# Performance work log

Measured on AMD Instinct MI355X. Metric: run time of the kernel, lower is better.

## Reference

```python
import jax, jax.numpy as jnp
import numpy as np

N, C, K = 65536, 128, 16

def setup_inputs() -> dict:
    key = jax.random.key(0)
    ks = jax.random.split(key, 16)
    def w(k, i, o):
        return jax.random.normal(k, (i, o), dtype=jnp.float32) / np.sqrt(i)
    inp = {
        "x": jax.random.normal(ks[0], (N, C), dtype=jnp.float32),
        "coords": jax.random.normal(ks[1], (N, 3), dtype=jnp.float32) * 10.0,
        "neighbor_idx": jax.random.randint(ks[2], (N, K), 0, N, dtype=jnp.int32),
        # linear_top / linear_down (1x1 Minkowski convs, BN folded into affine)
        "W_top": w(ks[3], C, C), "b_top": jnp.zeros((C,), jnp.float32),
        "W_down": w(ks[4], C, C), "b_down": jnp.zeros((C,), jnp.float32),
        # phi (query), psi (key), alpha (value) 1x1 convs
        "W_phi": w(ks[5], C, C), "b_phi": jnp.zeros((C,), jnp.float32),
        "W_psi": w(ks[6], C, C), "b_psi": jnp.zeros((C,), jnp.float32),
        "W_alpha": w(ks[7], C, C), "b_alpha": jnp.zeros((C,), jnp.float32),
        # delta: positional-encoding MLP on relative xyz (3 -> C -> C)
        "W_d1": w(ks[8], 3, C), "b_d1": jnp.zeros((C,), jnp.float32),
        "W_d2": w(ks[9], C, C), "b_d2": jnp.zeros((C,), jnp.float32),
        # gamma: attention MLP (C -> C -> C), vector attention
        "W_g1": w(ks[10], C, C), "b_g1": jnp.zeros((C,), jnp.float32),
        "W_g2": w(ks[11], C, C), "b_g2": jnp.zeros((C,), jnp.float32),
    }
    return inp

def reference(x, coords, W_top, b_top, W_down, b_down, W_phi, b_phi, W_psi, b_psi,
              W_alpha, b_alpha, W_d1, b_d1, W_d2, b_d2, W_g1, b_g1, W_g2, b_g2,
              neighbor_idx):
    # linear_top
    h = x @ W_top + b_top                                  # (N, C)
    phi = h @ W_phi + b_phi                                # (N, C) query
    psi = h @ W_psi + b_psi                                # (N, C) key
    alpha = h @ W_alpha + b_alpha                          # (N, C) value
    # gather neighbor features / coords (irregular access)
    nb_psi = psi[neighbor_idx]                             # (N, K, C)
    nb_alpha = alpha[neighbor_idx]                         # (N, K, C)
    rel = coords[:, None, :] - coords[neighbor_idx]        # (N, K, 3)
    # delta: relative positional encoding MLP
    pos = jax.nn.relu(rel @ W_d1 + b_d1) @ W_d2 + b_d2     # (N, K, C)
    # vector attention: gamma(phi_i - psi_j + delta)
    attn_in = phi[:, None, :] - nb_psi + pos               # (N, K, C)
    logits = jax.nn.relu(attn_in @ W_g1 + b_g1) @ W_g2 + b_g2
    w = jax.nn.softmax(logits, axis=1)                     # softmax over K neighbors
    y = jnp.sum(w * (nb_alpha + pos), axis=1)              # (N, C)
    # linear_down + residual
    return y @ W_down + b_down + x
```

## Files before the change

kernel.cpp:

```cpp
#include <hip/hip_runtime.h>
#include <math.h>

#define C 128
#define K 16
#define M 4
#define ROWS 64

typedef unsigned short ushort_t;
typedef unsigned int u32;
typedef float f32x4 __attribute__((ext_vector_type(4)));
typedef _Float16 f16x8 __attribute__((ext_vector_type(8)));

union U8h { _Float16 h[8]; uint4 u; };

__device__ __forceinline__ float f16tof(ushort_t b) {
    _Float16 h = __builtin_bit_cast(_Float16, b); return (float)h;
}
__device__ __forceinline__ ushort_t ftof16(float f) {
    _Float16 h = (_Float16)f; return __builtin_bit_cast(ushort_t, h);
}
__device__ __forceinline__ f32x4 mfma16(f16x8 a, f16x8 b, f32x4 c) {
    return __builtin_amdgcn_mfma_f32_16x16x32_f16(a, b, c, 0, 0, 0);
}

__global__ __launch_bounds__(128) void k_prep(
    const float* __restrict__ s0, const float* __restrict__ s1,
    const float* __restrict__ s2, const float* __restrict__ s3,
    ushort_t* __restrict__ d0, ushort_t* __restrict__ d1,
    ushort_t* __restrict__ d2, ushort_t* __restrict__ d3)
{
    const int m = blockIdx.x >> 7, n = blockIdx.x & 127, e = threadIdx.x;
    const float* s = (m==0) ? s0 : (m==1) ? s1 : (m==2) ? s2 : s3;
    ushort_t*   d = (m==0) ? d0 : (m==1) ? d1 : (m==2) ? d2 : d3;
    d[n*C + e] = ftof16(s[e*C + n]);
}

__global__ __launch_bounds__(512) void k_qkv2(
    const float* __restrict__ x,
    const ushort_t* __restrict__ WTt, const float* __restrict__ bt,
    const ushort_t* __restrict__ WTp, const float* __restrict__ bp,
    const ushort_t* __restrict__ WTs, const float* __restrict__ bs,
    const ushort_t* __restrict__ WTa, const float* __restrict__ ba,
    ushort_t* __restrict__ phiB, ushort_t* __restrict__ psiB,
    ushort_t* __restrict__ alfB)
{
    __shared__ ushort_t sX[64*C];
    __shared__ ushort_t sH[64*C];
    const int tid = threadIdx.x, lane = tid & 63, wv = tid >> 6;
    const int ncol = (wv<<4) + (lane&15), arow = lane&15;
    const int kgrp = lane>>4, krow0 = kgrp<<3;
    const int r0 = blockIdx.x * 64;

    {
        const int rX = tid>>3, cX = (tid&7)<<4;
        const float* xp = &x[(size_t)(r0+rX)*C + cX];
        #pragma unroll
        for (int hf = 0; hf < 2; ++hf) {
            const float4 a  = *(const float4*)&xp[hf*8 + 0];
            const float4 b2 = *(const float4*)&xp[hf*8 + 4];
            U8h v;
            v.h[0]=(_Float16)a.x;  v.h[1]=(_Float16)a.y;
            v.h[2]=(_Float16)a.z;  v.h[3]=(_Float16)a.w;
            v.h[4]=(_Float16)b2.x; v.h[5]=(_Float16)b2.y;
            v.h[6]=(_Float16)b2.z; v.h[7]=(_Float16)b2.w;
            const int col = cX + hf*8;
            *(uint4*)&sX[(rX<<7) + (col ^ ((rX&7)<<3))] = v.u;
        }
    }
    __syncthreads();

    {
        f16x8 bf[4]; f32x4 hacc[4];
        #pragma unroll
        for (int kk = 0; kk < 4; ++kk)
            bf[kk] = *(const f16x8*)&WTt[(size_t)ncol*C + (kk<<5) + krow0];
        #pragma unroll
        for (int m = 0; m < 4; ++m) hacc[m] = (f32x4){0.f,0.f,0.f,0.f};
        __builtin_amdgcn_s_setprio(1);
        #pragma unroll
        for (int m = 0; m < 4; ++m)
            #pragma unroll
            for (int kk = 0; kk < 4; ++kk) {
                const int row = (m<<4) + arow;
                const f16x8 af = *(const f16x8*)&sX[(row<<7) + (((kk<<5)+krow0) ^ ((arow&7)<<3))];
                hacc[m] = mfma16(af, bf[kk], hacc[m]);
            }
        __builtin_amdgcn_s_setprio(0);
        const float btc = bt[ncol];
        #pragma unroll
        for (int m = 0; m < 4; ++m)
            #pragma unroll
            for (int r = 0; r < 4; ++r) {
                const int row = (m<<4) + (kgrp<<2) + r;
                const u32 hv = ftof16(hacc[m][r] + btc);
                const u32 pv = (u32)__shfl_xor((int)hv, 1);
                if (!(lane&1))
                    *(u32*)&sH[(row<<7) + (ncol ^ ((row&7)<<3))] = hv | (pv<<16);
            }
    }
    __syncthreads();

#define OGEMM(WT_, b_, o_)                                                    \
    {                                                                         \
        f16x8 wf[4]; f32x4 oacc[4];                                           \
        _Pragma("unroll")                                                     \
        for (int kk = 0; kk < 4; ++kk)                                        \
            wf[kk] = *(const f16x8*)&WT_[(size_t)ncol*C + (kk<<5) + krow0];   \
        _Pragma("unroll")                                                     \
        for (int m = 0; m < 4; ++m) oacc[m] = (f32x4){0.f,0.f,0.f,0.f};      \
        __builtin_amdgcn_s_setprio(1);                                        \
        _Pragma("unroll")                                                     \
        for (int m = 0; m < 4; ++m)                                           \
            _Pragma("unroll")                                                 \
            for (int kk = 0; kk < 4; ++kk) {                                  \
                const int row = (m<<4) + arow;                                \
                const f16x8 af = *(const f16x8*)&sH[(row<<7) + (((kk<<5)+krow0) ^ ((arow&7)<<3))]; \
                oacc[m] = mfma16(af, wf[kk], oacc[m]);                        \
            }                                                                 \
        __builtin_amdgcn_s_setprio(0);                                        \
        const float bc = b_[ncol];                                            \
        _Pragma("unroll")                                                     \
        for (int m = 0; m < 4; ++m)                                           \
            _Pragma("unroll")                                                 \
            for (int r = 0; r < 4; ++r) {                                     \
                const int row = (m<<4) + (kgrp<<2) + r;                       \
                const u32 hv = ftof16(oacc[m][r] + bc);                       \
                const u32 pv = (u32)__shfl_xor((int)hv, 1);                   \
                if (!(lane&1))                                                \
                    *(u32*)&o_[(size_t)(r0+row)*C + ncol] = hv | (pv<<16);    \
            }                                                                 \
    }
    OGEMM(WTp, bp, phiB)
    OGEMM(WTs, bs, psiB)
    OGEMM(WTa, ba, alfB)
#undef OGEMM
}

__global__ __launch_bounds__(512, 2) void k_attn5(
    const ushort_t* __restrict__ phiB, const ushort_t* __restrict__ psiB,
    const ushort_t* __restrict__ alfB,
    const float* __restrict__ coords, const int* __restrict__ nidx,
    const float* __restrict__ Wd1, const float* __restrict__ bd1,
    const ushort_t* __restrict__ WTd2, const float* __restrict__ bd2,
    const ushort_t* __restrict__ WTg1, const float* __restrict__ bg1,
    const ushort_t* __restrict__ WTg2,
    const ushort_t* __restrict__ WTdn, const float* __restrict__ bdn,
    const float* __restrict__ x, float* __restrict__ out,
    int ngroups, int gpb)
{
    __shared__ ushort_t sT0[ROWS*C];
    __shared__ ushort_t sT1[ROWS*C];
    __shared__ ushort_t sA[ROWS*C];
    __shared__ float    sWd1[3][C];
    __shared__ float    sbd1v[C];
    __shared__ float    sY[M][C];

    const int tid  = threadIdx.x, lane = tid & 63, wv = tid >> 6;
    const int ncol = (wv<<4) + (lane&15);
    const int arow = lane & 15;
    const int kgrp = lane >> 4, krow0 = kgrp << 3;
    const int grow = tid >> 3;
    const int gpt  = grow >> 4;
    const int gk   = grow & 15;
    const int gc   = (tid & 7) << 4;

    const int g0 = blockIdx.x * gpb;
    if (g0 >= ngroups) return;
    const int gend = (g0 + gpb < ngroups) ? (g0 + gpb) : ngroups;

    if (tid < 3*C) ((float*)sWd1)[tid] = Wd1[tid];
    else if (tid < 4*C) sbd1v[tid - 3*C] = bd1[tid - 3*C];

    f16x8 wd2[4], wg1[4], wg2[4], wdn[4];
    #pragma unroll
    for (int kk = 0; kk < 4; ++kk) {
        wd2[kk] = *(const f16x8*)&WTd2[(size_t)ncol*C + (kk<<5) + krow0];
        wg1[kk] = *(const f16x8*)&WTg1[(size_t)ncol*C + (kk<<5) + krow0];
        wg2[kk] = *(const f16x8*)&WTg2[(size_t)ncol*C + (kk<<5) + krow0];
        wdn[kk] = *(const f16x8*)&WTdn[(size_t)ncol*C + (kgrp<<5) + (kk<<3)];
    }
    const float bd2c = bd2[ncol], bg1c = bg1[ncol], bdnc = bdn[ncol];

    __syncthreads();

    int jP; float cn0,cn1,cn2,cj0,cj1,cj2;
    {
        const int pt = g0*M + gpt;
        jP  = nidx[(size_t)pt*K + gk];
        cn0 = coords[(size_t)pt*3+0]; cn1 = coords[(size_t)pt*3+1]; cn2 = coords[(size_t)pt*3+2];
        cj0 = coords[(size_t)jP*3+0]; cj1 = coords[(size_t)jP*3+1]; cj2 = coords[(size_t)jP*3+2];
    }

    const int si0 = (grow<<7) + (gc ^ ((grow&7)<<3));
    const int si1 = (grow<<7) + ((gc+8) ^ ((grow&7)<<3));

    for (int g = g0; g < gend; ++g) {
        const int p0 = g * M;
        const bool hn = (g + 1 < gend);

        {
            const float rx = cn0 - cj0, ry = cn1 - cj1, rz = cn2 - cj2;
            #pragma unroll
            for (int hf = 0; hf < 2; ++hf) {
                U8h hi, lo;
                #pragma unroll
                for (int z = 0; z < 8; ++z) {
                    const int c = gc + (hf<<3) + z;
                    float t = fmaf(rx, sWd1[0][c],
                              fmaf(ry, sWd1[1][c],
                              fmaf(rz, sWd1[2][c], sbd1v[c])));
                    t = fmaxf(t, 0.f);
                    hi.h[z] = (_Float16)t;
                    lo.h[z] = (_Float16)(t - (float)hi.h[z]);
                }
                const int si = hf ? si1 : si0;
                *(uint4*)&sT0[si] = hi.u;
                *(uint4*)&sT1[si] = lo.u;
            }
        }
        __syncthreads();

        ushort_t phv[M];
        ushort_t psv[M][4];
        #pragma unroll
        for (int m = 0; m < M; ++m) {
            phv[m] = phiB[(size_t)(p0+m)*C + ncol];
            #pragma unroll
            for (int r = 0; r < 4; ++r) {
                const int j = nidx[(size_t)(p0+m)*K + (kgrp<<2) + r];
                psv[m][r] = psiB[(size_t)j*C + ncol];
            }
        }

        f32x4 pos[M];
        #pragma unroll
        for (int m = 0; m < M; ++m) pos[m] = (f32x4){0.f,0.f,0.f,0.f};
        __builtin_amdgcn_s_setprio(1);
        #pragma unroll
        for (int m = 0; m < M; ++m)
            #pragma unroll
            for (int kk = 0; kk < 4; ++kk) {
                const int si = (((m<<4)+arow)<<7) + (((kk<<5)+krow0) ^ ((arow&7)<<3));
                pos[m] = mfma16(*(const f16x8*)&sT0[si], wd2[kk], pos[m]);
                pos[m] = mfma16(*(const f16x8*)&sT1[si], wd2[kk], pos[m]);
            }
        __builtin_amdgcn_s_setprio(0);

        #pragma unroll
        for (int m = 0; m < M; ++m) {
            #pragma unroll
            for (int z = 0; z < 4; ++z) pos[m][z] += bd2c;
            const float phic = f16tof(phv[m]);
            #pragma unroll
            for (int r = 0; r < 4; ++r) {
                const int row = (m<<4) + (kgrp<<2) + r;
                const float av = phic - f16tof(psv[m][r]) + pos[m][r];
                const u32 hv = ftof16(av);
                const u32 hp = (u32)__shfl_xor((int)hv, 1);
                if (!(lane&1)) {
                    const int si = (row<<7) + (ncol ^ ((row&7)<<3));
                    *(u32*)&sA[si] = hv | (hp<<16);
                }
            }
        }
        __syncthreads();

        ushort_t alv[M][4];
        #pragma unroll
        for (int m = 0; m < M; ++m)
            #pragma unroll
            for (int r = 0; r < 4; ++r) {
                const int j = nidx[(size_t)(p0+m)*K + (kgrp<<2) + r];
                alv[m][r] = alfB[(size_t)j*C + ncol];
            }

        {
            f32x4 ua[M];
            #pragma unroll
            for (int m = 0; m < M; ++m) ua[m] = (f32x4){0.f,0.f,0.f,0.f};
            __builtin_amdgcn_s_setprio(1);
            #pragma unroll
            for (int m = 0; m < M; ++m)
                #pragma unroll
                for (int kk = 0; kk < 4; ++kk) {
                    const int si = (((m<<4)+arow)<<7) + (((kk<<5)+krow0) ^ ((arow&7)<<3));
                    ua[m] = mfma16(*(const f16x8*)&sA[si], wg1[kk], ua[m]);
                }
            __builtin_amdgcn_s_setprio(0);
            #pragma unroll
            for (int m = 0; m < M; ++m)
                #pragma unroll
                for (int r = 0; r < 4; ++r) {
                    const int row = (m<<4) + (kgrp<<2) + r;
                    const u32 hv = ftof16(fmaxf(ua[m][r] + bg1c, 0.f));
                    const u32 hp = (u32)__shfl_xor((int)hv, 1);
                    if (!(lane&1)) {
                        const int si = (row<<7) + (ncol ^ ((row&7)<<3));
                        *(u32*)&sT1[si] = hv | (hp<<16);
                    }
                }
        }
        if (hn) {
            const int pt = (g+1)*M + gpt;
            jP  = nidx[(size_t)pt*K + gk];
            cn0 = coords[(size_t)pt*3+0]; cn1 = coords[(size_t)pt*3+1]; cn2 = coords[(size_t)pt*3+2];
            cj0 = coords[(size_t)jP*3+0]; cj1 = coords[(size_t)jP*3+1]; cj2 = coords[(size_t)jP*3+2];
        }
        __syncthreads();

        f32x4 lg[M];
        #pragma unroll
        for (int m = 0; m < M; ++m) lg[m] = (f32x4){0.f,0.f,0.f,0.f};
        __builtin_amdgcn_s_setprio(1);
        #pragma unroll
        for (int m = 0; m < M; ++m)
            #pragma unroll
            for (int kk = 0; kk < 4; ++kk) {
                const int si = (((m<<4)+arow)<<7) + (((kk<<5)+krow0) ^ ((arow&7)<<3));
                lg[m] = mfma16(*(const f16x8*)&sT1[si], wg2[kk], lg[m]);
            }
        __builtin_amdgcn_s_setprio(0);

        #pragma unroll
        for (int m = 0; m < M; ++m) {
            float mx = fmaxf(fmaxf(lg[m][0], lg[m][1]), fmaxf(lg[m][2], lg[m][3]));
            mx = fmaxf(mx, __shfl_xor(mx, 16));
            mx = fmaxf(mx, __shfl_xor(mx, 32));
            const float e0 = __expf(lg[m][0]-mx), e1 = __expf(lg[m][1]-mx);
            const float e2 = __expf(lg[m][2]-mx), e3 = __expf(lg[m][3]-mx);
            float den = e0 + e1 + e2 + e3;
            den += __shfl_xor(den, 16);
            den += __shfl_xor(den, 32);
            const float inv = 1.0f / den;
            float yp;
            yp  = e0 * (f16tof(alv[m][0]) + pos[m][0]);
            yp += e1 * (f16tof(alv[m][1]) + pos[m][1]);
            yp += e2 * (f16tof(alv[m][2]) + pos[m][2]);
            yp += e3 * (f16tof(alv[m][3]) + pos[m][3]);
            yp *= inv;
            yp += __shfl_xor(yp, 16);
            yp += __shfl_xor(yp, 32);
            if (lane < 16) sY[m][ncol] = yp;
        }
        __syncthreads();

        #pragma unroll
        for (int m = 0; m < M; ++m) {
            float acc = 0.f;
            const int e0i = kgrp << 5;
            #pragma unroll
            for (int z = 0; z < 4; ++z) {
                const float4 ya = *(const float4*)&sY[m][e0i + (z<<3)];
                const float4 yb = *(const float4*)&sY[m][e0i + (z<<3) + 4];
                const f16x8 w8 = wdn[z];
                acc = fmaf(ya.x, (float)w8[0], acc);
                acc = fmaf(ya.y, (float)w8[1], acc);
                acc = fmaf(ya.z, (float)w8[2], acc);
                acc = fmaf(ya.w, (float)w8[3], acc);
                acc = fmaf(yb.x, (float)w8[4], acc);
                acc = fmaf(yb.y, (float)w8[5], acc);
                acc = fmaf(yb.z, (float)w8[6], acc);
                acc = fmaf(yb.w, (float)w8[7], acc);
            }
            acc += __shfl_xor(acc, 16);
            acc += __shfl_xor(acc, 32);
            if (lane < 16) {
                const size_t p = (size_t)(p0 + m);
                out[p*C + ncol] = acc + bdnc + x[p*C + ncol];
            }
        }
    }
}

extern "C" void kernel_launch(void* const* d_in, const int* in_sizes, int n_in,
                              void* d_out, int out_size, void* d_ws, size_t ws_size,
                              hipStream_t stream)
{
    const float* x      = (const float*)d_in[0];
    const float* coords = (const float*)d_in[1];
    const int*   nidx   = (const int*)d_in[2];
    const float* W_top  = (const float*)d_in[3];
    const float* b_top  = (const float*)d_in[4];
    const float* W_down = (const float*)d_in[5];
    const float* b_down = (const float*)d_in[6];
    const float* W_phi  = (const float*)d_in[7];
    const float* b_phi  = (const float*)d_in[8];
    const float* W_psi  = (const float*)d_in[9];
    const float* b_psi  = (const float*)d_in[10];
    const float* W_alpha= (const float*)d_in[11];
    const float* b_alpha= (const float*)d_in[12];
    const float* W_d1   = (const float*)d_in[13];
    const float* b_d1   = (const float*)d_in[14];
    const float* W_d2   = (const float*)d_in[15];
    const float* b_d2   = (const float*)d_in[16];
    const float* W_g1   = (const float*)d_in[17];
    const float* b_g1   = (const float*)d_in[18];
    const float* W_g2   = (const float*)d_in[19];
    const float* b_g2   = (const float*)d_in[20];
    (void)b_g2;

    const int N = in_sizes[0] / C;

    ushort_t* WTt  = (ushort_t*)d_ws;
    ushort_t* WTp  = WTt  + C*C;
    ushort_t* WTs  = WTp  + C*C;
    ushort_t* WTa  = WTs  + C*C;
    ushort_t* WTd2 = WTa  + C*C;
    ushort_t* WTg1 = WTd2 + C*C;
    ushort_t* WTg2 = WTg1 + C*C;
    ushort_t* WTdn = WTg2 + C*C;
    ushort_t* phiB = WTdn + C*C;
    ushort_t* psiB = phiB + (size_t)N*C;
    ushort_t* alfB = psiB + (size_t)N*C;
    float* out = (float*)d_out;

    hipLaunchKernelGGL(k_prep, dim3(4*C), dim3(C), 0, stream,
        W_top, W_phi, W_psi, W_alpha, WTt, WTp, WTs, WTa);
    hipLaunchKernelGGL(k_prep, dim3(4*C), dim3(C), 0, stream,
        W_d2, W_g1, W_g2, W_down, WTd2, WTg1, WTg2, WTdn);

    hipLaunchKernelGGL(k_qkv2, dim3(N / 64), dim3(512), 0, stream,
        x, WTt, b_top, WTp, b_phi, WTs, b_psi, WTa, b_alpha,
        phiB, psiB, alfB);

    const int ngroups = N / M;
    const int NBLK = 2048;
    const int gpb = (ngroups + NBLK - 1) / NBLK;
    hipLaunchKernelGGL(k_attn5, dim3(NBLK), dim3(512), 0, stream,
        phiB, psiB, alfB, coords, nidx,
        W_d1, b_d1, WTd2, b_d2, WTg1, b_g1, WTg2,
        WTdn, b_down, x, out, ngroups, gpb);
}
```

Before: 634.4 us.

## Split down-projection into separate MFMA kernel to cut attention kernel registers

```diff
diff --git a/kernel.cpp b/kernel.cpp
--- a/kernel.cpp
+++ b/kernel.cpp
@@ -92,10 +92,7 @@
             #pragma unroll
             for (int r = 0; r < 4; ++r) {
                 const int row = (m<<4) + (kgrp<<2) + r;
-                const u32 hv = ftof16(hacc[m][r] + btc);
-                const u32 pv = (u32)__shfl_xor((int)hv, 1);
-                if (!(lane&1))
-                    *(u32*)&sH[(row<<7) + (ncol ^ ((row&7)<<3))] = hv | (pv<<16);
+                sH[(row<<7) + (ncol ^ ((row&7)<<3))] = ftof16(hacc[m][r] + btc);
             }
     }
     __syncthreads();
@@ -124,10 +121,7 @@
             _Pragma("unroll")                                                 \
             for (int r = 0; r < 4; ++r) {                                     \
                 const int row = (m<<4) + (kgrp<<2) + r;                       \
-                const u32 hv = ftof16(oacc[m][r] + bc);                       \
-                const u32 pv = (u32)__shfl_xor((int)hv, 1);                   \
-                if (!(lane&1))                                                \
-                    *(u32*)&o_[(size_t)(r0+row)*C + ncol] = hv | (pv<<16);    \
+                o_[(size_t)(r0+row)*C + ncol] = ftof16(oacc[m][r] + bc);      \
             }                                                                 \
     }
     OGEMM(WTp, bp, phiB)
@@ -136,7 +130,7 @@
 #undef OGEMM
 }
 
-__global__ __launch_bounds__(512, 2) void k_attn5(
+__global__ __launch_bounds__(512, 4) void k_attn6(
     const ushort_t* __restrict__ phiB, const ushort_t* __restrict__ psiB,
     const ushort_t* __restrict__ alfB,
     const float* __restrict__ coords, const int* __restrict__ nidx,
@@ -144,8 +138,7 @@
     const ushort_t* __restrict__ WTd2, const float* __restrict__ bd2,
     const ushort_t* __restrict__ WTg1, const float* __restrict__ bg1,
     const ushort_t* __restrict__ WTg2,
-    const ushort_t* __restrict__ WTdn, const float* __restrict__ bdn,
-    const float* __restrict__ x, float* __restrict__ out,
+    ushort_t* __restrict__ yB,
     int ngroups, int gpb)
 {
     __shared__ ushort_t sT0[ROWS*C];
@@ -153,7 +146,6 @@
     __shared__ ushort_t sA[ROWS*C];
     __shared__ float    sWd1[3][C];
     __shared__ float    sbd1v[C];
-    __shared__ float    sY[M][C];
 
     const int tid  = threadIdx.x, lane = tid & 63, wv = tid >> 6;
     const int ncol = (wv<<4) + (lane&15);
@@ -171,15 +163,13 @@
     if (tid < 3*C) ((float*)sWd1)[tid] = Wd1[tid];
     else if (tid < 4*C) sbd1v[tid - 3*C] = bd1[tid - 3*C];
 
-    f16x8 wd2[4], wg1[4], wg2[4], wdn[4];
+    f16x8 wd2[4], wg1[4];
     #pragma unroll
     for (int kk = 0; kk < 4; ++kk) {
         wd2[kk] = *(const f16x8*)&WTd2[(size_t)ncol*C + (kk<<5) + krow0];
         wg1[kk] = *(const f16x8*)&WTg1[(size_t)ncol*C + (kk<<5) + krow0];
-        wg2[kk] = *(const f16x8*)&WTg2[(size_t)ncol*C + (kk<<5) + krow0];
-        wdn[kk] = *(const f16x8*)&WTdn[(size_t)ncol*C + (kgrp<<5) + (kk<<3)];
-    }
-    const float bd2c = bd2[ncol], bg1c = bg1[ncol], bdnc = bdn[ncol];
+    }
+    const float bd2c = bd2[ncol], bg1c = bg1[ncol];
 
     __syncthreads();
 
@@ -225,11 +215,11 @@
         #pragma unroll
         for (int m = 0; m < M; ++m) {
             phv[m] = phiB[(size_t)(p0+m)*C + ncol];
-            #pragma unroll
-            for (int r = 0; r < 4; ++r) {
-                const int j = nidx[(size_t)(p0+m)*K + (kgrp<<2) + r];
-                psv[m][r] = psiB[(size_t)j*C + ncol];
-            }
+            const int4 j4 = *(const int4*)&nidx[(size_t)(p0+m)*K + (kgrp<<2)];
+            psv[m][0] = psiB[(size_t)j4.x*C + ncol];
+            psv[m][1] = psiB[(size_t)j4.y*C + ncol];
+            psv[m][2] = psiB[(size_t)j4.z*C + ncol];
+            psv[m][3] = psiB[(size_t)j4.w*C + ncol];
         }
 
         f32x4 pos[M];
@@ -255,24 +245,24 @@
             for (int r = 0; r < 4; ++r) {
                 const int row = (m<<4) + (kgrp<<2) + r;
                 const float av = phic - f16tof(psv[m][r]) + pos[m][r];
-                const u32 hv = ftof16(av);
-                const u32 hp = (u32)__shfl_xor((int)hv, 1);
-                if (!(lane&1)) {
-                    const int si = (row<<7) + (ncol ^ ((row&7)<<3));
-                    *(u32*)&sA[si] = hv | (hp<<16);
-                }
+                sA[(row<<7) + (ncol ^ ((row&7)<<3))] = ftof16(av);
             }
         }
         __syncthreads();
 
         ushort_t alv[M][4];
         #pragma unroll
-        for (int m = 0; m < M; ++m)
-            #pragma unroll
-            for (int r = 0; r < 4; ++r) {
-                const int j = nidx[(size_t)(p0+m)*K + (kgrp<<2) + r];
-                alv[m][r] = alfB[(size_t)j*C + ncol];
-            }
+        for (int m = 0; m < M; ++m) {
+            const int4 j4 = *(const int4*)&nidx[(size_t)(p0+m)*K + (kgrp<<2)];
+            alv[m][0] = alfB[(size_t)j4.x*C + ncol];
+            alv[m][1] = alfB[(size_t)j4.y*C + ncol];
+            alv[m][2] = alfB[(size_t)j4.z*C + ncol];
+            alv[m][3] = alfB[(size_t)j4.w*C + ncol];
+        }
+        f16x8 wg2s[4];
+        #pragma unroll
+        for (int kk = 0; kk < 4; ++kk)
+            wg2s[kk] = *(const f16x8*)&WTg2[(size_t)ncol*C + (kk<<5) + krow0];
 
         {
             f32x4 ua[M];
@@ -292,12 +282,8 @@
                 #pragma unroll
                 for (int r = 0; r < 4; ++r) {
                     const int row = (m<<4) + (kgrp<<2) + r;
-                    const u32 hv = ftof16(fmaxf(ua[m][r] + bg1c, 0.f));
-                    const u32 hp = (u32)__shfl_xor((int)hv, 1);
-                    if (!(lane&1)) {
-                        const int si = (row<<7) + (ncol ^ ((row&7)<<3));
-                        *(u32*)&sT1[si] = hv | (hp<<16);
-                    }
+                    sT1[(row<<7) + (ncol ^ ((row&7)<<3))] =
+                        ftof16(fmaxf(ua[m][r] + bg1c, 0.f));
                 }
         }
         if (hn) {
@@ -317,7 +303,7 @@
             #pragma unroll
             for (int kk = 0; kk < 4; ++kk) {
                 const int si = (((m<<4)+arow)<<7) + (((kk<<5)+krow0) ^ ((arow&7)<<3));
-                lg[m] = mfma16(*(const f16x8*)&sT1[si], wg2[kk], lg[m]);
+                lg[m] = mfma16(*(const f16x8*)&sT1[si], wg2s[kk], lg[m]);
             }
         __builtin_amdgcn_s_setprio(0);
 
@@ -340,36 +326,59 @@
             yp *= inv;
             yp += __shfl_xor(yp, 16);
             yp += __shfl_xor(yp, 32);
-            if (lane < 16) sY[m][ncol] = yp;
+            if (lane < 16)
+                yB[(size_t)(p0+m)*C + ncol] = ftof16(yp);
         }
         __syncthreads();
-
-        #pragma unroll
-        for (int m = 0; m < M; ++m) {
-            float acc = 0.f;
-            const int e0i = kgrp << 5;
-            #pragma unroll
-            for (int z = 0; z < 4; ++z) {
-                const float4 ya = *(const float4*)&sY[m][e0i + (z<<3)];
-                const float4 yb = *(const float4*)&sY[m][e0i + (z<<3) + 4];
-                const f16x8 w8 = wdn[z];
-                acc = fmaf(ya.x, (float)w8[0], acc);
-                acc = fmaf(ya.y, (float)w8[1], acc);
-                acc = fmaf(ya.z, (float)w8[2], acc);
-                acc = fmaf(ya.w, (float)w8[3], acc);
-                acc = fmaf(yb.x, (float)w8[4], acc);
-                acc = fmaf(yb.y, (float)w8[5], acc);
-                acc = fmaf(yb.z, (float)w8[6], acc);
-                acc = fmaf(yb.w, (float)w8[7], acc);
-            }
-            acc += __shfl_xor(acc, 16);
-            acc += __shfl_xor(acc, 32);
-            if (lane < 16) {
-                const size_t p = (size_t)(p0 + m);
-                out[p*C + ncol] = acc + bdnc + x[p*C + ncol];
-            }
-        }
-    }
+    }
+}
+
+__global__ __launch_bounds__(512) void k_down(
+    const ushort_t* __restrict__ yB,
+    const ushort_t* __restrict__ WTdn, const float* __restrict__ bdn,
+    const float* __restrict__ x, float* __restrict__ out)
+{
+    __shared__ ushort_t sY[64*C];
+    const int tid = threadIdx.x, lane = tid & 63, wv = tid >> 6;
+    const int ncol = (wv<<4) + (lane&15), arow = lane&15;
+    const int kgrp = lane>>4, krow0 = kgrp<<3;
+    const int r0 = blockIdx.x * 64;
+
+    {
+        const int rY = tid>>3, cY = (tid&7)<<4;
+        #pragma unroll
+        for (int hf = 0; hf < 2; ++hf) {
+            const uint4 v = *(const uint4*)&yB[(size_t)(r0+rY)*C + cY + hf*8];
+            *(uint4*)&sY[(rY<<7) + ((cY + hf*8) ^ ((rY&7)<<3))] = v;
+        }
+    }
+    __syncthreads();
+
+    f16x8 wf[4]; f32x4 oacc[4];
+    #pragma unroll
+    for (int kk = 0; kk < 4; ++kk)
+        wf[kk] = *(const f16x8*)&WTdn[(size_t)ncol*C + (kk<<5) + krow0];
+    #pragma unroll
+    for (int m = 0; m < 4; ++m) oacc[m] = (f32x4){0.f,0.f,0.f,0.f};
+    __builtin_amdgcn_s_setprio(1);
+    #pragma unroll
+    for (int m = 0; m < 4; ++m)
+        #pragma unroll
+        for (int kk = 0; kk < 4; ++kk) {
+            const int row = (m<<4) + arow;
+            const f16x8 af = *(const f16x8*)&sY[(row<<7) + (((kk<<5)+krow0) ^ ((arow&7)<<3))];
+            oacc[m] = mfma16(af, wf[kk], oacc[m]);
+        }
+    __builtin_amdgcn_s_setprio(0);
+    const float bc = bdn[ncol];
+    #pragma unroll
+    for (int m = 0; m < 4; ++m)
+        #pragma unroll
+        for (int r = 0; r < 4; ++r) {
+            const int row = (m<<4) + (kgrp<<2) + r;
+            const size_t idx = (size_t)(r0+row)*C + ncol;
+            out[idx] = oacc[m][r] + bc + x[idx];
+        }
 }
 
 extern "C" void kernel_launch(void* const* d_in, const int* in_sizes, int n_in,
@@ -412,6 +421,7 @@
     ushort_t* phiB = WTdn + C*C;
     ushort_t* psiB = phiB + (size_t)N*C;
     ushort_t* alfB = psiB + (size_t)N*C;
+    ushort_t* yB   = alfB + (size_t)N*C;
     float* out = (float*)d_out;
 
     hipLaunchKernelGGL(k_prep, dim3(4*C), dim3(C), 0, stream,
@@ -426,8 +436,11 @@
     const int ngroups = N / M;
     const int NBLK = 2048;
     const int gpb = (ngroups + NBLK - 1) / NBLK;
-    hipLaunchKernelGGL(k_attn5, dim3(NBLK), dim3(512), 0, stream,
+    hipLaunchKernelGGL(k_attn6, dim3(NBLK), dim3(512), 0, stream,
         phiB, psiB, alfB, coords, nidx,
         W_d1, b_d1, WTd2, b_d2, WTg1, b_g1, WTg2,
-        WTdn, b_down, x, out, ngroups, gpb);
-}
+        yB, ngroups, gpb);
+
+    hipLaunchKernelGGL(k_down, dim3(N / 64), dim3(512), 0, stream,
+        yB, WTdn, b_down, x, out);
+}
```

New measurement: 542.2 us. 14.5% less time.
